# Kernel tuning notes

Measured on AMD Instinct MI355X. Metric: run time of the kernel, lower is better.

Reference implementation:

```python
import jax, jax.numpy as jnp
import numpy as np

EDGE_WIDTH = 128
NUM_HEADS = 8
DOT_DIM = EDGE_WIDTH // NUM_HEADS  # 16
B, N = 2, 256


def _layernorm(x, g, b, eps=1e-5):
    mu = jnp.mean(x, axis=-1, keepdims=True)
    var = jnp.var(x, axis=-1, keepdims=True)
    return (x - mu) * jax.lax.rsqrt(var + eps) * g + b


def setup_inputs() -> dict:
    key = jax.random.key(0)
    ks = jax.random.split(key, 8)
    W = EDGE_WIDTH
    H = NUM_HEADS
    s = lambda fan_in: 1.0 / np.sqrt(fan_in)
    return {
        "e": jax.random.normal(ks[0], (B, N, N, W), dtype=jnp.float32),
        "mask": jnp.zeros((B, N, N, 1), dtype=jnp.float32),
        "ln_g": jnp.ones((W,), dtype=jnp.float32),
        "ln_b": jnp.zeros((W,), dtype=jnp.float32),
        "W_V": jax.random.uniform(ks[1], (W, 2 * W), jnp.float32, -s(W), s(W)),
        "b_V": jnp.zeros((2 * W,), dtype=jnp.float32),
        "W_E": jax.random.uniform(ks[2], (W, 2 * H), jnp.float32, -s(W), s(W)),
        "b_E": jnp.zeros((2 * H,), dtype=jnp.float32),
        "W_O": jax.random.uniform(ks[3], (2 * W, W), jnp.float32, -s(2 * W), s(2 * W)),
        "b_O": jnp.zeros((W,), dtype=jnp.float32),
    }


def reference(e, mask, ln_g, ln_b, W_V, b_V, W_E, b_E, W_O, b_O):
    bsize, num_edges, _, embed_dim = e.shape
    H, D = NUM_HEADS, DOT_DIM

    e_ln = _layernorm(e, ln_g, ln_b)

    V = e_ln @ W_V + b_V                       # [B,N,N,2W]
    V_in, V_out = jnp.split(V, 2, axis=-1)     # each [B,N,N,W]
    V_in = V_in.reshape(bsize, num_edges, num_edges, D, H)
    V_out = V_out.reshape(bsize, num_edges, num_edges, D, H)

    E = e_ln @ W_E + b_E                       # [B,N,N,2H]
    E_in, E_out = jnp.split(E, 2, axis=-1)     # each [B,N,N,H]

    # NOTE: original module computes a scale factor but never applies it.
    A_in = jax.nn.softmax(E_in + mask, axis=2)            # softmax over k
    Va_in = jnp.einsum('bikh,bjkdh->bijdh', A_in, V_in)

    A_out = jax.nn.softmax(E_out + mask, axis=1)          # softmax over k
    Va_out = jnp.einsum('bkih,bkjdh->bijdh', A_out, V_out)

    Va = jnp.concatenate([Va_in, Va_out], axis=-1)        # [B,N,N,D,2H]
    Va = Va.reshape(bsize, num_edges, num_edges, embed_dim * 2)
    return Va @ W_O + b_O
```

## Files before the change

### kernel.cpp

```cpp
#include <hip/hip_runtime.h>
#include <hip/hip_bf16.h>
#include <stdint.h>


typedef short short8 __attribute__((ext_vector_type(8)));
typedef short short4v __attribute__((ext_vector_type(4)));
typedef float floatx4 __attribute__((ext_vector_type(4)));

#define AS1(p) ((const __attribute__((address_space(1))) void*)(p))
#define AS3(p) ((__attribute__((address_space(3))) void*)(p))

__device__ inline short f2bf(float v) {
    uint32_t u = __builtin_bit_cast(uint32_t, v);
    u += 0x7FFFu + ((u >> 16) & 1u);
    return (short)(u >> 16);
}

__global__ __launch_bounds__(128) void k0_prep(const float* __restrict__ WV,
                                               const float* __restrict__ WE,
                                               const float* __restrict__ WO,
                                               short* __restrict__ Wcat2,
                                               short* __restrict__ WOt,
                                               const float* __restrict__ bV,
                                               const float* __restrict__ bE,
                                               float* __restrict__ bcat) {
    int bx = blockIdx.x;
    if (bx < 288) {
        int v = bx / 144, n = bx % 144, k = threadIdx.x;
        float val = 0.f;
        if (n < 128) val = WV[k * 256 + v * 128 + n];
        else if (n < 136) val = WE[k * 16 + v * 8 + (n - 128)];
        Wcat2[(v * 144 + n) * 128 + k] = f2bf(val);
    } else if (bx < 416) {
        int w = bx - 288;
        for (int it = 0; it < 2; ++it) {
            int c = threadIdx.x + it * 128;
            float val = WO[((c & 15) * 16 + (c >> 4)) * 128 + w];
            WOt[w * 256 + c] = f2bf(val);
        }
    } else {
        for (int it = 0; it < 3; ++it) {
            int idx = it * 128 + threadIdx.x;
            if (idx < 288) {
                int v = idx / 144, n = idx % 144;
                float val = 0.f;
                if (n < 128) val = bV[v * 128 + n];
                else if (n < 136) val = bE[v * 8 + (n - 128)];
                bcat[idx] = val;
            }
        }
    }
}

__global__ __launch_bounds__(256, 2) void k1_ln_proj(
    const float* __restrict__ e, const float* __restrict__ ln_g,
    const float* __restrict__ ln_b, const float* __restrict__ mask,
    const short* __restrict__ Wcat2, const float* __restrict__ bcat,
    short* __restrict__ VinT, short* __restrict__ VoutT,
    short* __restrict__ Ain, short* __restrict__ AoutT) {
    __shared__ short At[256 * 128];
    __shared__ float maskb[256];
    __shared__ float redm[4][8];
    __shared__ float reds[4][8];

    const int tid = threadIdx.x;
    const int fix = blockIdx.x;
    const int b = blockIdx.y;
    const int v = blockIdx.z;
    const int estride = v ? 256 : 1;
    const size_t ebase = (size_t)b * 65536 + (size_t)fix * (v ? 1 : 256);
    const short* Wv = Wcat2 + v * 144 * 128;
    const float* bc = bcat + v * 144;
    short* Vdst = v ? VoutT : VinT;
    short* Adst = v ? AoutT : Ain;

    maskb[tid] = mask[(size_t)b * 65536 + (v ? (size_t)tid * 256 + fix
                                             : (size_t)fix * 256 + tid)];

    {
        const int rq = tid & 3;
        const int rowi = tid >> 2;
#pragma unroll
        for (int pass = 0; pass < 4; ++pass) {
            int row = pass * 64 + rowi;
            const float* ep = e + (ebase + (size_t)row * estride) * 128 + rq * 4;
            float4 val[8];
            float s = 0.f, s2 = 0.f;
#pragma unroll
            for (int i = 0; i < 8; ++i) {
                val[i] = *(const float4*)(ep + i * 16);
                s += val[i].x + val[i].y + val[i].z + val[i].w;
                s2 += val[i].x * val[i].x + val[i].y * val[i].y +
                      val[i].z * val[i].z + val[i].w * val[i].w;
            }
            s += __shfl_xor(s, 1); s2 += __shfl_xor(s2, 1);
            s += __shfl_xor(s, 2); s2 += __shfl_xor(s2, 2);
            float mean = s * 0.0078125f;
            float var = s2 * 0.0078125f - mean * mean;
            float rs = rsqrtf(var + 1e-5f);
#pragma unroll
            for (int i = 0; i < 8; ++i) {
                int col = i * 16 + rq * 4;
                float4 gg = *(const float4*)(ln_g + col);
                float4 bb = *(const float4*)(ln_b + col);
                short4v o;
                o[0] = f2bf((val[i].x - mean) * rs * gg.x + bb.x);
                o[1] = f2bf((val[i].y - mean) * rs * gg.y + bb.y);
                o[2] = f2bf((val[i].z - mean) * rs * gg.z + bb.z);
                o[3] = f2bf((val[i].w - mean) * rs * gg.w + bb.w);
                int g = col >> 3;
                int cp = g ^ (row & 15);
                int half = (col >> 2) & 1;
                *(short4v*)&At[row * 128 + cp * 8 + half * 4] = o;
            }
        }
    }
    __syncthreads();

    const int lane = tid & 63, w = tid >> 6;
    const int ln_ = lane & 15, quad = lane >> 4;

#pragma unroll
    for (int chunk = 0; chunk < 2; ++chunk) {
        floatx4 acc[4][4] = {};
#pragma unroll
        for (int kk = 0; kk < 4; ++kk) {
            int cp = (kk * 4 + quad) ^ ln_;
            short8 aq[4];
#pragma unroll
            for (int mt = 0; mt < 4; ++mt) {
                int r = w * 64 + mt * 16 + ln_;
                aq[mt] = *(const short8*)&At[r * 128 + cp * 8];
            }
            short8 bq[4];
#pragma unroll
            for (int ntl = 0; ntl < 4; ++ntl) {
                int n = chunk * 64 + ntl * 16 + ln_;
                bq[ntl] = *(const short8*)(Wv + n * 128 + (kk * 4 + quad) * 8);
            }
#pragma unroll
            for (int mt = 0; mt < 4; ++mt)
#pragma unroll
                for (int ntl = 0; ntl < 4; ++ntl)
                    acc[mt][ntl] = __builtin_amdgcn_mfma_f32_16x16x32_bf16(
                        aq[mt], bq[ntl], acc[mt][ntl], 0, 0, 0);
        }
#pragma unroll
        for (int ntl = 0; ntl < 4; ++ntl) {
            int c = chunk * 64 + ntl * 16 + ln_;
            float bias = bc[c];
            int d = c >> 3, hh = c & 7;
            size_t rowbase = (((size_t)(b * 8 + hh) * 256 + fix) * 16 + d) * 256;
#pragma unroll
            for (int mt = 0; mt < 4; ++mt) {
                short4v o;
#pragma unroll
                for (int r = 0; r < 4; ++r) o[r] = f2bf(acc[mt][ntl][r] + bias);
                *(short4v*)(Vdst + rowbase + w * 64 + mt * 16 + quad * 4) = o;
            }
        }
    }

    {
        floatx4 accE[4] = {};
        int n = 128 + ln_;
#pragma unroll
        for (int kk = 0; kk < 4; ++kk) {
            int cp = (kk * 4 + quad) ^ ln_;
            short8 bq = *(const short8*)(Wv + n * 128 + (kk * 4 + quad) * 8);
#pragma unroll
            for (int mt = 0; mt < 4; ++mt) {
                int r = w * 64 + mt * 16 + ln_;
                short8 aq = *(const short8*)&At[r * 128 + cp * 8];
                accE[mt] = __builtin_amdgcn_mfma_f32_16x16x32_bf16(
                    aq, bq, accE[mt], 0, 0, 0);
            }
        }
        float bias = bc[128 + ln_];
        float vE[16];
        float m = -3.4e38f;
#pragma unroll
        for (int mt = 0; mt < 4; ++mt)
#pragma unroll
            for (int r = 0; r < 4; ++r) {
                int k = w * 64 + mt * 16 + quad * 4 + r;
                float x = accE[mt][r] + bias + maskb[k];
                vE[mt * 4 + r] = x;
                m = fmaxf(m, x);
            }
        m = fmaxf(m, __shfl_xor(m, 16));
        m = fmaxf(m, __shfl_xor(m, 32));
        if (quad == 0 && ln_ < 8) redm[w][ln_] = m;
        __syncthreads();
        int hs = ln_ & 7;
        float bmax = fmaxf(fmaxf(redm[0][hs], redm[1][hs]),
                           fmaxf(redm[2][hs], redm[3][hs]));
        float p[16], s = 0.f;
#pragma unroll
        for (int i = 0; i < 16; ++i) { p[i] = __expf(vE[i] - bmax); s += p[i]; }
        s += __shfl_xor(s, 16);
        s += __shfl_xor(s, 32);
        if (quad == 0 && ln_ < 8) reds[w][ln_] = s;
        __syncthreads();
        float inv = 1.f / (reds[0][hs] + reds[1][hs] + reds[2][hs] + reds[3][hs]);
        if (ln_ < 8) {
            size_t rowbase = (size_t)(b * 8 + ln_) * 65536 + (size_t)fix * 256;
#pragma unroll
            for (int mt = 0; mt < 4; ++mt) {
                short4v o;
#pragma unroll
                for (int r = 0; r < 4; ++r) o[r] = f2bf(p[mt * 4 + r] * inv);
                *(short4v*)(Adst + rowbase + w * 64 + mt * 16 + quad * 4) = o;
            }
        }
    }
}

__global__ __launch_bounds__(256) void k3_einsum(const short* __restrict__ Ain,
                                                 const short* __restrict__ AoutT,
                                                 const short* __restrict__ VinT,
                                                 const short* __restrict__ VoutT,
                                                 short* __restrict__ VaP2) {
    __shared__ short AB[4096 * 8];
    const int tid = threadIdx.x, lane = tid & 63, w = tid >> 6;
    const int i0 = blockIdx.x * 128;
    const int jd0 = blockIdx.y * 128;
    const int z = blockIdx.z;
    const int b = z >> 4, part = (z >> 3) & 1, h = z & 7;

    const short* Abase = (part ? AoutT : Ain) + ((size_t)(b * 8 + h)) * 65536 + (size_t)i0 * 256;
    const short* Bbase = (part ? VoutT : VinT) + ((size_t)(b * 8 + h)) * 1048576 + (size_t)jd0 * 256;

    const int ln_ = lane & 15, quad = lane >> 4;
    const int m0 = (w >> 1) * 64, n0 = (w & 1) * 64;
    floatx4 acc[4][4] = {};

    for (int kt = 0; kt < 2; ++kt) {
        if (kt) __syncthreads();
        for (int it = 0; it < 16; ++it) {
            int cid = w * 1024 + it * 64 + lane;
            int isB = cid >> 11;
            int lc = cid & 2047;
            int r = lc >> 4;
            int ck = (lc & 15) ^ (r & 15);
            const short* g = (isB ? Bbase : Abase) + r * 256 + kt * 128 + ck * 8;
            __builtin_amdgcn_global_load_lds(AS1(g), AS3(&AB[cid * 8]), 16, 0, 0);
        }
        __syncthreads();

        for (int kk = 0; kk < 4; ++kk) {
            int ckb = kk * 4 + quad;
            short8 aq[4], bq[4];
#pragma unroll
            for (int t = 0; t < 4; ++t) {
                int r = m0 + t * 16 + ln_;
                aq[t] = *(const short8*)&AB[(r * 16 + (ckb ^ (r & 15))) * 8];
            }
#pragma unroll
            for (int t = 0; t < 4; ++t) {
                int r = n0 + t * 16 + ln_;
                bq[t] = *(const short8*)&AB[(2048 + r * 16 + (ckb ^ (r & 15))) * 8];
            }
#pragma unroll
            for (int mt = 0; mt < 4; ++mt)
#pragma unroll
                for (int nt = 0; nt < 4; ++nt)
                    acc[mt][nt] = __builtin_amdgcn_mfma_f32_16x16x32_bf16(aq[mt], bq[nt], acc[mt][nt], 0, 0, 0);
        }
    }

    const int ph = part * 8 + h;
#pragma unroll
    for (int mt = 0; mt < 4; ++mt) {
#pragma unroll
        for (int nt = 0; nt < 4; ++nt) {
            int j = (jd0 + n0 + nt * 16) >> 4;
#pragma unroll
            for (int r = 0; r < 4; ++r) {
                int i = i0 + m0 + mt * 16 + quad * 4 + r;
                size_t m = ((size_t)b * 256 + i) * 256 + j;
                VaP2[((size_t)ph * 131072 + m) * 16 + ln_] = f2bf(acc[mt][nt][r]);
            }
        }
    }
}

__global__ __launch_bounds__(256) void k4_proj(const short* __restrict__ VaP2,
                                               const short* __restrict__ WOt,
                                               const float* __restrict__ bO,
                                               float* __restrict__ out) {
    __shared__ short A_s[16384];
    const int tid = threadIdx.x, lane = tid & 63, w = tid >> 6;
    const size_t m0g = (size_t)blockIdx.x * 128;
    const int ln_ = lane & 15, quad = lane >> 4;
    const int m0 = (w >> 1) * 64, n0 = (w & 1) * 64;
    floatx4 acc[4][4] = {};

    for (int kt = 0; kt < 2; ++kt) {
        if (kt) __syncthreads();
        for (int it = 0; it < 8; ++it) {
            int cid = w * 512 + it * 64 + lane;
            int p = cid >> 8, rm = cid & 255, half = rm >> 7, m = rm & 127;
            const short* g = VaP2 + ((size_t)(kt * 8 + p) * 131072 + m0g + m) * 16 + half * 8;
            __builtin_amdgcn_global_load_lds(AS1(g), AS3(&A_s[cid * 8]), 16, 0, 0);
        }
        __syncthreads();

        for (int kk = 0; kk < 4; ++kk) {
            int ckb = kk * 4 + quad;
            int p = ckb >> 1, hf = ckb & 1;
            short8 aq[4], bq[4];
#pragma unroll
            for (int t = 0; t < 4; ++t) {
                int m = m0 + t * 16 + ln_;
                aq[t] = *(const short8*)&A_s[p * 2048 + hf * 1024 + m * 8];
            }
#pragma unroll
            for (int t = 0; t < 4; ++t) {
                int wr = n0 + t * 16 + ln_;
                bq[t] = *(const short8*)(WOt + wr * 256 + kt * 128 + ckb * 8);
            }
#pragma unroll
            for (int mt = 0; mt < 4; ++mt)
#pragma unroll
                for (int nt = 0; nt < 4; ++nt)
                    acc[mt][nt] = __builtin_amdgcn_mfma_f32_16x16x32_bf16(aq[mt], bq[nt], acc[mt][nt], 0, 0, 0);
        }
    }

#pragma unroll
    for (int nt = 0; nt < 4; ++nt) {
        int ww = n0 + nt * 16 + ln_;
        float bo = bO[ww];
#pragma unroll
        for (int mt = 0; mt < 4; ++mt) {
            size_t mb = m0g + m0 + mt * 16 + quad * 4;
#pragma unroll
            for (int r = 0; r < 4; ++r)
                out[(mb + r) * 128 + ww] = acc[mt][nt][r] + bo;
        }
    }
}

extern "C" void kernel_launch(void* const* d_in, const int* in_sizes, int n_in,
                              void* d_out, int out_size, void* d_ws, size_t ws_size,
                              hipStream_t stream) {
    (void)in_sizes; (void)n_in; (void)out_size; (void)ws_size;
    const float* e    = (const float*)d_in[0];
    const float* mask = (const float*)d_in[1];
    const float* ln_g = (const float*)d_in[2];
    const float* ln_b = (const float*)d_in[3];
    const float* W_V  = (const float*)d_in[4];
    const float* b_V  = (const float*)d_in[5];
    const float* W_E  = (const float*)d_in[6];
    const float* b_E  = (const float*)d_in[7];
    const float* W_O  = (const float*)d_in[8];
    const float* b_O  = (const float*)d_in[9];
    float* out = (float*)d_out;

    char* ws = (char*)d_ws;
    short* VinT  = (short*)(ws + 0);
    short* VoutT = (short*)(ws + 33554432);
    short* Ain   = (short*)(ws + 67108864);
    short* AoutT = (short*)(ws + 69206016);
    short* VaP2  = (short*)(ws + 71303168);
    short* Wcat2 = (short*)(ws + 138412032);
    short* WOt   = (short*)(ws + 138485760);
    float* bcat  = (float*)(ws + 138551296);

    k0_prep<<<417, 128, 0, stream>>>(W_V, W_E, W_O, Wcat2, WOt, b_V, b_E, bcat);
    k1_ln_proj<<<dim3(256, 2, 2), 256, 0, stream>>>(e, ln_g, ln_b, mask, Wcat2,
                                                    bcat, VinT, VoutT, Ain, AoutT);
    k3_einsum<<<dim3(2, 32, 32), 256, 0, stream>>>(Ain, AoutT, VinT, VoutT, VaP2);
    k4_proj<<<1024, 256, 0, stream>>>(VaP2, WOt, b_O, out);
}
```

Before: 245.8 us.

## Halve LDS tiles in LN-projection and einsum kernels, relayout weights for coalesced reads

The LN+projection kernel now processes its 256 rows in two halves with a 128-row LDS tile, cutting shared memory from 64KB so more blocks can be resident (launch bound raised to 4). The einsum kernel splits K into four 64-wide steps with a 32KB tile and a launch bound of 3. The weight matrices are re-laid out k-chunk-major so that the 16-byte fragment loads of adjacent lanes are contiguous in memory, and the MFMA inner loops are unrolled. The cost is more barriers and loop iterations per block, plus serialized load/compute phases that may limit latency hiding.

Result: slower. 312.5 us (+27.2%).

```diff
diff --git a/kernel.cpp b/kernel.cpp
--- a/kernel.cpp
+++ b/kernel.cpp
@@ -19,28 +19,32 @@
 __global__ __launch_bounds__(128) void k0_prep(const float* __restrict__ WV,
                                                const float* __restrict__ WE,
                                                const float* __restrict__ WO,
-                                               short* __restrict__ Wcat2,
-                                               short* __restrict__ WOt,
+                                               short* __restrict__ Wk,
+                                               short* __restrict__ WOt2,
                                                const float* __restrict__ bV,
                                                const float* __restrict__ bE,
                                                float* __restrict__ bcat) {
-    int bx = blockIdx.x;
-    if (bx < 288) {
-        int v = bx / 144, n = bx % 144, k = threadIdx.x;
-        float val = 0.f;
-        if (n < 128) val = WV[k * 256 + v * 128 + n];
-        else if (n < 136) val = WE[k * 16 + v * 8 + (n - 128)];
-        Wcat2[(v * 144 + n) * 128 + k] = f2bf(val);
-    } else if (bx < 416) {
-        int w = bx - 288;
-        for (int it = 0; it < 2; ++it) {
-            int c = threadIdx.x + it * 128;
-            float val = WO[((c & 15) * 16 + (c >> 4)) * 128 + w];
-            WOt[w * 256 + c] = f2bf(val);
+    int bx = blockIdx.x, t = threadIdx.x;
+    if (bx < 32) {
+        int v = bx >> 4, kc = bx & 15;
+        for (int it = 0; it < 9; ++it) {
+            int idx = it * 128 + t;
+            int n = idx >> 3, j = idx & 7, k = kc * 8 + j;
+            float val = 0.f;
+            if (n < 128) val = WV[k * 256 + v * 128 + n];
+            else if (n < 136) val = WE[k * 16 + v * 8 + (n - 128)];
+            Wk[((v * 16 + kc) * 144 + n) * 8 + j] = f2bf(val);
+        }
+    } else if (bx < 64) {
+        int cc = bx - 32;
+        for (int j = 0; j < 8; ++j) {
+            int c = cc * 8 + j;
+            WOt2[(cc * 128 + t) * 8 + j] =
+                f2bf(WO[((c & 15) * 16 + (c >> 4)) * 128 + t]);
         }
     } else {
         for (int it = 0; it < 3; ++it) {
-            int idx = it * 128 + threadIdx.x;
+            int idx = it * 128 + t;
             if (idx < 288) {
                 int v = idx / 144, n = idx % 144;
                 float val = 0.f;
@@ -52,13 +56,13 @@
     }
 }
 
-__global__ __launch_bounds__(256, 2) void k1_ln_proj(
+__global__ __launch_bounds__(256, 4) void k1_ln_proj(
     const float* __restrict__ e, const float* __restrict__ ln_g,
     const float* __restrict__ ln_b, const float* __restrict__ mask,
-    const short* __restrict__ Wcat2, const float* __restrict__ bcat,
+    const short* __restrict__ Wk, const float* __restrict__ bcat,
     short* __restrict__ VinT, short* __restrict__ VoutT,
     short* __restrict__ Ain, short* __restrict__ AoutT) {
-    __shared__ short At[256 * 128];
+    __shared__ short At[128 * 128];
     __shared__ float maskb[256];
     __shared__ float redm[4][8];
     __shared__ float reds[4][8];
@@ -69,7 +73,7 @@
     const int v = blockIdx.z;
     const int estride = v ? 256 : 1;
     const size_t ebase = (size_t)b * 65536 + (size_t)fix * (v ? 1 : 256);
-    const short* Wv = Wcat2 + v * 144 * 128;
+    const short* Wv = Wk + v * 16 * 144 * 8;
     const float* bc = bcat + v * 144;
     short* Vdst = v ? VoutT : VinT;
     short* Adst = v ? AoutT : Ain;
@@ -77,117 +81,126 @@
     maskb[tid] = mask[(size_t)b * 65536 + (v ? (size_t)tid * 256 + fix
                                              : (size_t)fix * 256 + tid)];
 
-    {
-        const int rq = tid & 3;
-        const int rowi = tid >> 2;
-#pragma unroll
-        for (int pass = 0; pass < 4; ++pass) {
-            int row = pass * 64 + rowi;
-            const float* ep = e + (ebase + (size_t)row * estride) * 128 + rq * 4;
-            float4 val[8];
-            float s = 0.f, s2 = 0.f;
-#pragma unroll
-            for (int i = 0; i < 8; ++i) {
-                val[i] = *(const float4*)(ep + i * 16);
-                s += val[i].x + val[i].y + val[i].z + val[i].w;
-                s2 += val[i].x * val[i].x + val[i].y * val[i].y +
-                      val[i].z * val[i].z + val[i].w * val[i].w;
-            }
-            s += __shfl_xor(s, 1); s2 += __shfl_xor(s2, 1);
-            s += __shfl_xor(s, 2); s2 += __shfl_xor(s2, 2);
-            float mean = s * 0.0078125f;
-            float var = s2 * 0.0078125f - mean * mean;
-            float rs = rsqrtf(var + 1e-5f);
-#pragma unroll
-            for (int i = 0; i < 8; ++i) {
-                int col = i * 16 + rq * 4;
-                float4 gg = *(const float4*)(ln_g + col);
-                float4 bb = *(const float4*)(ln_b + col);
-                short4v o;
-                o[0] = f2bf((val[i].x - mean) * rs * gg.x + bb.x);
-                o[1] = f2bf((val[i].y - mean) * rs * gg.y + bb.y);
-                o[2] = f2bf((val[i].z - mean) * rs * gg.z + bb.z);
-                o[3] = f2bf((val[i].w - mean) * rs * gg.w + bb.w);
-                int g = col >> 3;
-                int cp = g ^ (row & 15);
-                int half = (col >> 2) & 1;
-                *(short4v*)&At[row * 128 + cp * 8 + half * 4] = o;
-            }
-        }
-    }
-    __syncthreads();
-
     const int lane = tid & 63, w = tid >> 6;
     const int ln_ = lane & 15, quad = lane >> 4;
-
-#pragma unroll
-    for (int chunk = 0; chunk < 2; ++chunk) {
-        floatx4 acc[4][4] = {};
-#pragma unroll
-        for (int kk = 0; kk < 4; ++kk) {
-            int cp = (kk * 4 + quad) ^ ln_;
-            short8 aq[4];
-#pragma unroll
-            for (int mt = 0; mt < 4; ++mt) {
-                int r = w * 64 + mt * 16 + ln_;
-                aq[mt] = *(const short8*)&At[r * 128 + cp * 8];
-            }
-            short8 bq[4];
+    float vE[16];
+
+    for (int hl = 0; hl < 2; ++hl) {
+        if (hl) __syncthreads();
+        {
+            const int rq = tid & 3;
+            const int rowi = tid >> 2;
+#pragma unroll
+            for (int pass = 0; pass < 2; ++pass) {
+                int row = pass * 64 + rowi;
+                int krow = hl * 128 + row;
+                const float* ep = e + (ebase + (size_t)krow * estride) * 128 + rq * 4;
+                float4 val[8];
+                float s = 0.f, s2 = 0.f;
+#pragma unroll
+                for (int i = 0; i < 8; ++i) {
+                    val[i] = *(const float4*)(ep + i * 16);
+                    s += val[i].x + val[i].y + val[i].z + val[i].w;
+                    s2 += val[i].x * val[i].x + val[i].y * val[i].y +
+                          val[i].z * val[i].z + val[i].w * val[i].w;
+                }
+                s += __shfl_xor(s, 1); s2 += __shfl_xor(s2, 1);
+                s += __shfl_xor(s, 2); s2 += __shfl_xor(s2, 2);
+                float mean = s * 0.0078125f;
+                float var = s2 * 0.0078125f - mean * mean;
+                float rs = rsqrtf(var + 1e-5f);
+#pragma unroll
+                for (int i = 0; i < 8; ++i) {
+                    int col = i * 16 + rq * 4;
+                    float4 gg = *(const float4*)(ln_g + col);
+                    float4 bb = *(const float4*)(ln_b + col);
+                    short4v o;
+                    o[0] = f2bf((val[i].x - mean) * rs * gg.x + bb.x);
+                    o[1] = f2bf((val[i].y - mean) * rs * gg.y + bb.y);
+                    o[2] = f2bf((val[i].z - mean) * rs * gg.z + bb.z);
+                    o[3] = f2bf((val[i].w - mean) * rs * gg.w + bb.w);
+                    int g = col >> 3;
+                    int cp = g ^ (row & 15);
+                    int hf4 = (col >> 2) & 1;
+                    *(short4v*)&At[row * 128 + cp * 8 + hf4 * 4] = o;
+                }
+            }
+        }
+        __syncthreads();
+
+#pragma unroll
+        for (int chunk = 0; chunk < 2; ++chunk) {
+            floatx4 acc[2][4] = {};
+#pragma unroll
+            for (int kk = 0; kk < 4; ++kk) {
+                int ckb = kk * 4 + quad;
+                int cp = ckb ^ ln_;
+                short8 aq[2];
+#pragma unroll
+                for (int mt = 0; mt < 2; ++mt) {
+                    int r = w * 32 + mt * 16 + ln_;
+                    aq[mt] = *(const short8*)&At[r * 128 + cp * 8];
+                }
+                short8 bq[4];
+#pragma unroll
+                for (int ntl = 0; ntl < 4; ++ntl) {
+                    int n = chunk * 64 + ntl * 16 + ln_;
+                    bq[ntl] = *(const short8*)(Wv + (ckb * 144 + n) * 8);
+                }
+#pragma unroll
+                for (int mt = 0; mt < 2; ++mt)
+#pragma unroll
+                    for (int ntl = 0; ntl < 4; ++ntl)
+                        acc[mt][ntl] = __builtin_amdgcn_mfma_f32_16x16x32_bf16(
+                            aq[mt], bq[ntl], acc[mt][ntl], 0, 0, 0);
+            }
 #pragma unroll
             for (int ntl = 0; ntl < 4; ++ntl) {
-                int n = chunk * 64 + ntl * 16 + ln_;
-                bq[ntl] = *(const short8*)(Wv + n * 128 + (kk * 4 + quad) * 8);
-            }
-#pragma unroll
-            for (int mt = 0; mt < 4; ++mt)
-#pragma unroll
-                for (int ntl = 0; ntl < 4; ++ntl)
-                    acc[mt][ntl] = __builtin_amdgcn_mfma_f32_16x16x32_bf16(
-                        aq[mt], bq[ntl], acc[mt][ntl], 0, 0, 0);
-        }
-#pragma unroll
-        for (int ntl = 0; ntl < 4; ++ntl) {
-            int c = chunk * 64 + ntl * 16 + ln_;
-            float bias = bc[c];
-            int d = c >> 3, hh = c & 7;
-            size_t rowbase = (((size_t)(b * 8 + hh) * 256 + fix) * 16 + d) * 256;
-#pragma unroll
-            for (int mt = 0; mt < 4; ++mt) {
-                short4v o;
-#pragma unroll
-                for (int r = 0; r < 4; ++r) o[r] = f2bf(acc[mt][ntl][r] + bias);
-                *(short4v*)(Vdst + rowbase + w * 64 + mt * 16 + quad * 4) = o;
-            }
+                int c = chunk * 64 + ntl * 16 + ln_;
+                float bias = bc[c];
+                int d = c >> 3, hh = c & 7;
+                size_t rowbase = (((size_t)(b * 8 + hh) * 256 + fix) * 16 + d) * 256;
+#pragma unroll
+                for (int mt = 0; mt < 2; ++mt) {
+                    short4v o;
+#pragma unroll
+                    for (int r = 0; r < 4; ++r) o[r] = f2bf(acc[mt][ntl][r] + bias);
+                    *(short4v*)(Vdst + rowbase + hl * 128 + w * 32 + mt * 16 + quad * 4) = o;
+                }
+            }
+        }
+
+        {
+            floatx4 accE[2] = {};
+            int n = 128 + ln_;
+#pragma unroll
+            for (int kk = 0; kk < 4; ++kk) {
+                int ckb = kk * 4 + quad;
+                int cp = ckb ^ ln_;
+                short8 bq = *(const short8*)(Wv + (ckb * 144 + n) * 8);
+#pragma unroll
+                for (int mt = 0; mt < 2; ++mt) {
+                    int r = w * 32 + mt * 16 + ln_;
+                    short8 aq = *(const short8*)&At[r * 128 + cp * 8];
+                    accE[mt] = __builtin_amdgcn_mfma_f32_16x16x32_bf16(
+                        aq, bq, accE[mt], 0, 0, 0);
+                }
+            }
+            float bias = bc[128 + ln_];
+#pragma unroll
+            for (int mt = 0; mt < 2; ++mt)
+#pragma unroll
+                for (int r = 0; r < 4; ++r) {
+                    int k = hl * 128 + w * 32 + mt * 16 + quad * 4 + r;
+                    vE[hl * 8 + mt * 4 + r] = accE[mt][r] + bias + maskb[k];
+                }
         }
     }
 
     {
-        floatx4 accE[4] = {};
-        int n = 128 + ln_;
-#pragma unroll
-        for (int kk = 0; kk < 4; ++kk) {
-            int cp = (kk * 4 + quad) ^ ln_;
-            short8 bq = *(const short8*)(Wv + n * 128 + (kk * 4 + quad) * 8);
-#pragma unroll
-            for (int mt = 0; mt < 4; ++mt) {
-                int r = w * 64 + mt * 16 + ln_;
-                short8 aq = *(const short8*)&At[r * 128 + cp * 8];
-                accE[mt] = __builtin_amdgcn_mfma_f32_16x16x32_bf16(
-                    aq, bq, accE[mt], 0, 0, 0);
-            }
-        }
-        float bias = bc[128 + ln_];
-        float vE[16];
-        float m = -3.4e38f;
-#pragma unroll
-        for (int mt = 0; mt < 4; ++mt)
-#pragma unroll
-            for (int r = 0; r < 4; ++r) {
-                int k = w * 64 + mt * 16 + quad * 4 + r;
-                float x = accE[mt][r] + bias + maskb[k];
-                vE[mt * 4 + r] = x;
-                m = fmaxf(m, x);
-            }
+        float m = vE[0];
+#pragma unroll
+        for (int i = 1; i < 16; ++i) m = fmaxf(m, vE[i]);
         m = fmaxf(m, __shfl_xor(m, 16));
         m = fmaxf(m, __shfl_xor(m, 32));
         if (quad == 0 && ln_ < 8) redm[w][ln_] = m;
@@ -206,22 +219,25 @@
         if (ln_ < 8) {
             size_t rowbase = (size_t)(b * 8 + ln_) * 65536 + (size_t)fix * 256;
 #pragma unroll
-            for (int mt = 0; mt < 4; ++mt) {
-                short4v o;
-#pragma unroll
-                for (int r = 0; r < 4; ++r) o[r] = f2bf(p[mt * 4 + r] * inv);
-                *(short4v*)(Adst + rowbase + w * 64 + mt * 16 + quad * 4) = o;
-            }
-        }
-    }
-}
-
-__global__ __launch_bounds__(256) void k3_einsum(const short* __restrict__ Ain,
-                                                 const short* __restrict__ AoutT,
-                                                 const short* __restrict__ VinT,
-                                                 const short* __restrict__ VoutT,
-                                                 short* __restrict__ VaP2) {
-    __shared__ short AB[4096 * 8];
+            for (int hl = 0; hl < 2; ++hl)
+#pragma unroll
+                for (int mt = 0; mt < 2; ++mt) {
+                    short4v o;
+#pragma unroll
+                    for (int r = 0; r < 4; ++r)
+                        o[r] = f2bf(p[hl * 8 + mt * 4 + r] * inv);
+                    *(short4v*)(Adst + rowbase + hl * 128 + w * 32 + mt * 16 + quad * 4) = o;
+                }
+        }
+    }
+}
+
+__global__ __launch_bounds__(256, 3) void k3_einsum(const short* __restrict__ Ain,
+                                                    const short* __restrict__ AoutT,
+                                                    const short* __restrict__ VinT,
+                                                    const short* __restrict__ VoutT,
+                                                    short* __restrict__ VaP2) {
+    __shared__ short AB[2048 * 8];
     const int tid = threadIdx.x, lane = tid & 63, w = tid >> 6;
     const int i0 = blockIdx.x * 128;
     const int jd0 = blockIdx.y * 128;
@@ -235,31 +251,32 @@
     const int m0 = (w >> 1) * 64, n0 = (w & 1) * 64;
     floatx4 acc[4][4] = {};
 
-    for (int kt = 0; kt < 2; ++kt) {
+    for (int kt = 0; kt < 4; ++kt) {
         if (kt) __syncthreads();
-        for (int it = 0; it < 16; ++it) {
-            int cid = w * 1024 + it * 64 + lane;
-            int isB = cid >> 11;
-            int lc = cid & 2047;
-            int r = lc >> 4;
-            int ck = (lc & 15) ^ (r & 15);
-            const short* g = (isB ? Bbase : Abase) + r * 256 + kt * 128 + ck * 8;
+        for (int it = 0; it < 8; ++it) {
+            int cid = w * 512 + it * 64 + lane;
+            int isB = cid >> 10;
+            int lc = cid & 1023;
+            int r = lc >> 3;
+            int ck = (lc & 7) ^ (r & 7);
+            const short* g = (isB ? Bbase : Abase) + r * 256 + kt * 64 + ck * 8;
             __builtin_amdgcn_global_load_lds(AS1(g), AS3(&AB[cid * 8]), 16, 0, 0);
         }
         __syncthreads();
 
-        for (int kk = 0; kk < 4; ++kk) {
+#pragma unroll
+        for (int kk = 0; kk < 2; ++kk) {
             int ckb = kk * 4 + quad;
             short8 aq[4], bq[4];
 #pragma unroll
             for (int t = 0; t < 4; ++t) {
                 int r = m0 + t * 16 + ln_;
-                aq[t] = *(const short8*)&AB[(r * 16 + (ckb ^ (r & 15))) * 8];
+                aq[t] = *(const short8*)&AB[(r * 8 + (ckb ^ (r & 7))) * 8];
             }
 #pragma unroll
             for (int t = 0; t < 4; ++t) {
                 int r = n0 + t * 16 + ln_;
-                bq[t] = *(const short8*)&AB[(2048 + r * 16 + (ckb ^ (r & 15))) * 8];
+                bq[t] = *(const short8*)&AB[(1024 + r * 8 + (ckb ^ (r & 7))) * 8];
             }
 #pragma unroll
             for (int mt = 0; mt < 4; ++mt)
@@ -285,10 +302,10 @@
     }
 }
 
-__global__ __launch_bounds__(256) void k4_proj(const short* __restrict__ VaP2,
-                                               const short* __restrict__ WOt,
-                                               const float* __restrict__ bO,
-                                               float* __restrict__ out) {
+__global__ __launch_bounds__(256, 3) void k4_proj(const short* __restrict__ VaP2,
+                                                  const short* __restrict__ WOt2,
+                                                  const float* __restrict__ bO,
+                                                  float* __restrict__ out) {
     __shared__ short A_s[16384];
     const int tid = threadIdx.x, lane = tid & 63, w = tid >> 6;
     const size_t m0g = (size_t)blockIdx.x * 128;
@@ -306,6 +323,7 @@
         }
         __syncthreads();
 
+#pragma unroll
         for (int kk = 0; kk < 4; ++kk) {
             int ckb = kk * 4 + quad;
             int p = ckb >> 1, hf = ckb & 1;
@@ -318,7 +336,7 @@
 #pragma unroll
             for (int t = 0; t < 4; ++t) {
                 int wr = n0 + t * 16 + ln_;
-                bq[t] = *(const short8*)(WOt + wr * 256 + kt * 128 + ckb * 8);
+                bq[t] = *(const short8*)(WOt2 + ((kt * 16 + ckb) * 128 + wr) * 8);
             }
 #pragma unroll
             for (int mt = 0; mt < 4; ++mt)
@@ -364,13 +382,13 @@
     short* Ain   = (short*)(ws + 67108864);
     short* AoutT = (short*)(ws + 69206016);
     short* VaP2  = (short*)(ws + 71303168);
-    short* Wcat2 = (short*)(ws + 138412032);
-    short* WOt   = (short*)(ws + 138485760);
+    short* Wk    = (short*)(ws + 138412032);
+    short* WOt2  = (short*)(ws + 138485760);
     float* bcat  = (float*)(ws + 138551296);
 
-    k0_prep<<<417, 128, 0, stream>>>(W_V, W_E, W_O, Wcat2, WOt, b_V, b_E, bcat);
-    k1_ln_proj<<<dim3(256, 2, 2), 256, 0, stream>>>(e, ln_g, ln_b, mask, Wcat2,
+    k0_prep<<<65, 128, 0, stream>>>(W_V, W_E, W_O, Wk, WOt2, b_V, b_E, bcat);
+    k1_ln_proj<<<dim3(256, 2, 2), 256, 0, stream>>>(e, ln_g, ln_b, mask, Wk,
                                                     bcat, VinT, VoutT, Ain, AoutT);
     k3_einsum<<<dim3(2, 32, 32), 256, 0, stream>>>(Ain, AoutT, VinT, VoutT, VaP2);
-    k4_proj<<<1024, 256, 0, stream>>>(VaP2, WOt, b_O, out);
-}
+    k4_proj<<<1024, 256, 0, stream>>>(VaP2, WOt2, b_O, out);
+}
```
